# Kernel tuning notes

Hardware: AMD Instinct MI355X
Metric: run time of the kernel (lower is better)

Reference implementation:

```python
import jax, jax.numpy as jnp
import numpy as np

B, S, DM, H, D = 2, 1024, 1024, 16, 64  # batch, seq, d_model, heads, head_dim


def setup_inputs() -> dict:
    key = jax.random.key(0)
    ks = jax.random.split(key, 16)
    sc = 1.0 / np.sqrt(DM)
    scd = 1.0 / np.sqrt(D)
    return {
        "hidden_states": jax.random.normal(ks[0], (B, S, DM), dtype=jnp.float32),
        # frozen base_attn projections
        "Wq": jax.random.normal(ks[1], (DM, DM), dtype=jnp.float32) * sc,
        "bq": jnp.zeros((DM,), dtype=jnp.float32),
        "Wk": jax.random.normal(ks[2], (DM, DM), dtype=jnp.float32) * sc,
        "bk": jnp.zeros((DM,), dtype=jnp.float32),
        "Wv": jax.random.normal(ks[3], (DM, DM), dtype=jnp.float32) * sc,
        "bv": jnp.zeros((DM,), dtype=jnp.float32),
        "Wo": jax.random.normal(ks[4], (DM, DM), dtype=jnp.float32) * sc,
        "bo": jnp.zeros((DM,), dtype=jnp.float32),
        # trainable hedgehog feature maps (per-head Linear(head_dim, head_dim))
        "Wfq": jax.random.normal(ks[5], (D, D), dtype=jnp.float32) * scd,
        "bfq": jnp.zeros((D,), dtype=jnp.float32),
        "Wfk": jax.random.normal(ks[6], (D, D), dtype=jnp.float32) * scd,
        "bfk": jnp.zeros((D,), dtype=jnp.float32),
    }


def _heads(x):
    # (B, S, DM) -> (B, H, S, D)
    return x.reshape(B, S, H, D).transpose(0, 2, 1, 3)


def _feature_map(x, W, b):
    # HedgehogFeatureMap: Linear then concat(exp(x), exp(-x)) along last dim
    y = jnp.einsum('bhsd,ed->bhse', x, W) + b
    return jnp.concatenate([jnp.exp(y), jnp.exp(-y)], axis=-1)  # (B,H,S,2D)


def reference(hidden_states, Wq, bq, Wk, bk, Wv, bv, Wo, bo, Wfq, bfq, Wfk, bfk):
    # base_attn: standard multi-head softmax attention with output_attentions=True
    q = _heads(hidden_states @ Wq.T + bq)
    k = _heads(hidden_states @ Wk.T + bk)
    v = _heads(hidden_states @ Wv.T + bv)
    scores = jnp.einsum('bhmd,bhnd->bhmn', q, k) / jnp.sqrt(jnp.float32(D))
    true_attns = jax.nn.softmax(scores, axis=-1)  # (B,H,S,S)
    ctx = jnp.einsum('bhmn,bhnd->bhmd', true_attns, v)
    outputs = ctx.transpose(0, 2, 1, 3).reshape(B, S, DM) @ Wo.T + bo

    # hedgehog path: feature maps on q/k then sum-normalized quadratic attention
    fq = _feature_map(q, Wfq, bfq)
    fk = _feature_map(k, Wfk, bfk)
    qk = jnp.einsum('bhmd,bhnd->bhmn', fq, fk)
    pred_attns = qk / jnp.sum(qk, axis=-1, keepdims=True)
    return (outputs, pred_attns, true_attns)
```

## Files before the change

kernel.cpp:

```cpp
#include <hip/hip_runtime.h>
#include <math.h>

constexpr int B_ = 2, S_ = 1024, DM_ = 1024, NH_ = 16, HD_ = 64;
constexpr long SD = (long)S_ * DM_;
constexpr long SS = (long)S_ * S_;

typedef _Float16 half8 __attribute__((ext_vector_type(8)));
typedef _Float16 half4 __attribute__((ext_vector_type(4)));
typedef float floatx4 __attribute__((ext_vector_type(4)));

__device__ __forceinline__ void gl_lds16(const void* g, void* l) {
    __builtin_amdgcn_global_load_lds(
        (const __attribute__((address_space(1))) void*)g,
        (__attribute__((address_space(3))) void*)l, 16, 0, 0);
}

__global__ __launch_bounds__(256) void cvt_f2h(
    const float* __restrict__ x, _Float16* __restrict__ y, int n4)
{
    int i = (blockIdx.x * 256 + threadIdx.x);
    if (i < n4) {
        float4 v = ((const float4*)x)[i];
        half4 h = { (_Float16)v.x, (_Float16)v.y, (_Float16)v.z, (_Float16)v.w };
        ((half4*)y)[i] = h;
    }
}

template <int BM, int BN, int WM, int WN, int CONVA>
__global__ __launch_bounds__(256) void mm_nt(
    const void* __restrict__ Ap, const _Float16* __restrict__ Wp,
    const float* __restrict__ bias, const float* __restrict__ rowscale,
    float* __restrict__ Cf,
    _Float16* __restrict__ Ch, int K, int lda, int ldw, int ldc,
    long sAb, long sAh, long sWb, long sWh, long sCb, long sCh,
    float scale, int mode)
{
    constexpr int MI = WM / 16, NI = WN / 16;
    const int z = blockIdx.z, b = z / NH_, h = z % NH_;
    const int wave = threadIdx.x >> 6, lane = threadIdx.x & 63;
    const int m0 = blockIdx.y * BM, n0 = blockIdx.x * BN;
    const int wm = (wave >> 1) * WM, wn = (wave & 1) * WN;
    const int r16 = lane & 15, quad = lane >> 4;

    const _Float16* Wz = Wp + (long)b * sWb + (long)h * sWh;

    __shared__ __align__(16) _Float16 As[BM * 32];
    __shared__ __align__(16) _Float16 Bs[BN * 32];

    floatx4 acc[MI][NI];
#pragma unroll
    for (int i = 0; i < MI; ++i)
#pragma unroll
        for (int j = 0; j < NI; ++j)
#pragma unroll
            for (int r = 0; r < 4; ++r) acc[i][j][r] = 0.f;

    for (int k0 = 0; k0 < K; k0 += 32) {
        if constexpr (CONVA) {
            const float* Af = (const float*)Ap + (long)b * sAb + (long)h * sAh;
#pragma unroll
            for (int r = 0; r < BM / 32; ++r) {
                int idx = r * 1024 + threadIdx.x * 4;
                int row = idx >> 5, col = idx & 31;
                float4 v = *(const float4*)(Af + (long)(m0 + row) * lda + k0 + col);
                half4 hv = { (_Float16)v.x, (_Float16)v.y, (_Float16)v.z, (_Float16)v.w };
                *(half4*)&As[row * 32 + col] = hv;
            }
        } else {
            const _Float16* Ah = (const _Float16*)Ap + (long)b * sAb + (long)h * sAh;
#pragma unroll
            for (int c = wave * (BM / 64); c < (wave + 1) * (BM / 64); ++c) {
                const _Float16* g = Ah + (long)(m0 + c * 16 + (lane >> 2)) * lda
                                    + k0 + (lane & 3) * 8;
                gl_lds16(g, &As[c * 512]);
            }
        }
#pragma unroll
        for (int c = wave * (BN / 64); c < (wave + 1) * (BN / 64); ++c) {
            const _Float16* g = Wz + (long)(n0 + c * 16 + (lane >> 2)) * ldw
                                + k0 + (lane & 3) * 8;
            gl_lds16(g, &Bs[c * 512]);
        }
        __syncthreads();

        half8 af[MI], bf8[NI];
#pragma unroll
        for (int i = 0; i < MI; ++i)
            af[i] = *(const half8*)&As[(wm + i * 16 + r16) * 32 + quad * 8];
#pragma unroll
        for (int j = 0; j < NI; ++j)
            bf8[j] = *(const half8*)&Bs[(wn + j * 16 + r16) * 32 + quad * 8];
#pragma unroll
        for (int i = 0; i < MI; ++i)
#pragma unroll
            for (int j = 0; j < NI; ++j)
                acc[i][j] = __builtin_amdgcn_mfma_f32_16x16x32_f16(
                    af[i], bf8[j], acc[i][j], 0, 0, 0);
        __syncthreads();
    }

    const long cb = (long)b * sCb + (long)h * sCh;
#pragma unroll
    for (int i = 0; i < MI; ++i) {
#pragma unroll
        for (int j = 0; j < NI; ++j) {
#pragma unroll
            for (int r = 0; r < 4; ++r) {
                int row = m0 + wm + i * 16 + quad * 4 + r;
                int col = n0 + wn + j * 16 + r16;
                float v = acc[i][j][r] * scale;
                if (bias) v += bias[col];
                if (rowscale) v *= rowscale[(long)z * 1024 + row];
                if (mode == 0) Cf[cb + (long)row * ldc + col] = v;
                else           Ch[cb + (long)row * ldc + col] = (_Float16)v;
            }
        }
    }
}

__global__ __launch_bounds__(256) void qkv_proj(
    const _Float16* __restrict__ hsH,
    const _Float16* __restrict__ W0, const _Float16* __restrict__ W1,
    const _Float16* __restrict__ W2,
    const float* __restrict__ b0, const float* __restrict__ b1,
    const float* __restrict__ b2,
    _Float16* __restrict__ QH, _Float16* __restrict__ KH,
    _Float16* __restrict__ VtH)
{
    const int z = blockIdx.z;
    const _Float16* W = (z == 0) ? W0 : (z == 1) ? W1 : W2;
    const float* bias = (z == 0) ? b0 : (z == 1) ? b1 : b2;

    const int wave = threadIdx.x >> 6, lane = threadIdx.x & 63;
    const int m0 = blockIdx.y * 128, n0 = blockIdx.x * 128;
    const int wm = (wave >> 1) * 64, wn = (wave & 1) * 64;
    const int r16 = lane & 15, quad = lane >> 4;

    __shared__ __align__(16) _Float16 As[128 * 32];
    __shared__ __align__(16) _Float16 Bs[128 * 32];

    floatx4 acc[4][4];
#pragma unroll
    for (int i = 0; i < 4; ++i)
#pragma unroll
        for (int j = 0; j < 4; ++j)
#pragma unroll
            for (int r = 0; r < 4; ++r) acc[i][j][r] = 0.f;

    for (int k0 = 0; k0 < 1024; k0 += 32) {
#pragma unroll
        for (int c = wave * 2; c < wave * 2 + 2; ++c) {
            const _Float16* ga = hsH + (long)(m0 + c * 16 + (lane >> 2)) * 1024
                                 + k0 + (lane & 3) * 8;
            gl_lds16(ga, &As[c * 512]);
            const _Float16* gb = W + (long)(n0 + c * 16 + (lane >> 2)) * 1024
                                 + k0 + (lane & 3) * 8;
            gl_lds16(gb, &Bs[c * 512]);
        }
        __syncthreads();

        half8 af[4], bf8[4];
#pragma unroll
        for (int i = 0; i < 4; ++i)
            af[i] = *(const half8*)&As[(wm + i * 16 + r16) * 32 + quad * 8];
#pragma unroll
        for (int j = 0; j < 4; ++j)
            bf8[j] = *(const half8*)&Bs[(wn + j * 16 + r16) * 32 + quad * 8];
#pragma unroll
        for (int i = 0; i < 4; ++i)
#pragma unroll
            for (int j = 0; j < 4; ++j)
                acc[i][j] = __builtin_amdgcn_mfma_f32_16x16x32_f16(
                    af[i], bf8[j], acc[i][j], 0, 0, 0);
        __syncthreads();
    }

    _Float16* dst = (z == 0) ? QH : KH;
#pragma unroll
    for (int i = 0; i < 4; ++i) {
#pragma unroll
        for (int j = 0; j < 4; ++j) {
#pragma unroll
            for (int r = 0; r < 4; ++r) {
                int row = m0 + wm + i * 16 + quad * 4 + r;
                int col = n0 + wn + j * 16 + r16;
                float v = acc[i][j][r] + bias[col];
                if (z < 2) {
                    dst[(long)row * 1024 + col] = (_Float16)v;
                } else {
                    int bb = row >> 10, s = row & 1023;
                    int hh = col >> 6, d = col & 63;
                    VtH[((((long)bb * 16 + hh) * 64 + d) << 10) | s] = (_Float16)v;
                }
            }
        }
    }
}

__global__ __launch_bounds__(512) void attn_fused(
    const _Float16* __restrict__ Q, const _Float16* __restrict__ K,
    const _Float16* __restrict__ Vt, float* __restrict__ trueA,
    _Float16* __restrict__ ctx)
{
    const int z = blockIdx.y, b = z >> 4, h = z & 15;
    const int m0 = blockIdx.x * 32;
    const int wave = threadIdx.x >> 6, lane = threadIdx.x & 63;
    const int r16 = lane & 15, quad = lane >> 4;
    const int c0 = wave * 128;

    __shared__ __align__(16) _Float16 Ps[32 * 1024];
    float* redmx = (float*)Ps;
    float* redsm = (float*)Ps + 256;
    float* kred  = (float*)Ps;

    const _Float16* Qb = Q + (long)b * SD + h * 64;
    const _Float16* Kb = K + (long)b * SD + h * 64;

    half8 af[2][2];
#pragma unroll
    for (int mi = 0; mi < 2; ++mi)
#pragma unroll
        for (int ks = 0; ks < 2; ++ks)
            af[mi][ks] = *(const half8*)&Qb[(long)(m0 + mi * 16 + r16) * DM_
                                            + ks * 32 + quad * 8];

    floatx4 acc[2][8];
#pragma unroll
    for (int mi = 0; mi < 2; ++mi)
#pragma unroll
        for (int nj = 0; nj < 8; ++nj)
#pragma unroll
            for (int r = 0; r < 4; ++r) acc[mi][nj][r] = 0.f;

#pragma unroll
    for (int ks = 0; ks < 2; ++ks) {
#pragma unroll
        for (int nj = 0; nj < 8; ++nj) {
            half8 bf = *(const half8*)&Kb[(long)(c0 + nj * 16 + r16) * DM_
                                          + ks * 32 + quad * 8];
            acc[0][nj] = __builtin_amdgcn_mfma_f32_16x16x32_f16(
                af[0][ks], bf, acc[0][nj], 0, 0, 0);
            acc[1][nj] = __builtin_amdgcn_mfma_f32_16x16x32_f16(
                af[1][ks], bf, acc[1][nj], 0, 0, 0);
        }
    }

    float rmx[2][4];
#pragma unroll
    for (int mi = 0; mi < 2; ++mi)
#pragma unroll
        for (int r = 0; r < 4; ++r) {
            float m = acc[mi][0][r];
#pragma unroll
            for (int nj = 1; nj < 8; ++nj) m = fmaxf(m, acc[mi][nj][r]);
#pragma unroll
            for (int o = 1; o <= 8; o <<= 1) m = fmaxf(m, __shfl_xor(m, o, 64));
            rmx[mi][r] = m;
        }
    if (r16 == 0) {
#pragma unroll
        for (int mi = 0; mi < 2; ++mi)
#pragma unroll
            for (int r = 0; r < 4; ++r)
                redmx[wave * 32 + mi * 16 + quad * 4 + r] = rmx[mi][r];
    }
    __syncthreads();
    float mx[2][4];
#pragma unroll
    for (int mi = 0; mi < 2; ++mi)
#pragma unroll
        for (int r = 0; r < 4; ++r) {
            float m = redmx[mi * 16 + quad * 4 + r];
#pragma unroll
            for (int w = 1; w < 8; ++w)
                m = fmaxf(m, redmx[w * 32 + mi * 16 + quad * 4 + r]);
            mx[mi][r] = m;
        }

    float rsm[2][4];
#pragma unroll
    for (int mi = 0; mi < 2; ++mi)
#pragma unroll
        for (int r = 0; r < 4; ++r) {
            float s = 0.f;
#pragma unroll
            for (int nj = 0; nj < 8; ++nj) {
                float p = __expf((acc[mi][nj][r] - mx[mi][r]) * 0.125f);
                acc[mi][nj][r] = p;
                s += p;
            }
#pragma unroll
            for (int o = 1; o <= 8; o <<= 1) s += __shfl_xor(s, o, 64);
            rsm[mi][r] = s;
        }
    if (r16 == 0) {
#pragma unroll
        for (int mi = 0; mi < 2; ++mi)
#pragma unroll
            for (int r = 0; r < 4; ++r)
                redsm[wave * 32 + mi * 16 + quad * 4 + r] = rsm[mi][r];
    }
    __syncthreads();
    float inv[2][4];
#pragma unroll
    for (int mi = 0; mi < 2; ++mi)
#pragma unroll
        for (int r = 0; r < 4; ++r) {
            float s = 0.f;
#pragma unroll
            for (int w = 0; w < 8; ++w)
                s += redsm[w * 32 + mi * 16 + quad * 4 + r];
            inv[mi][r] = 1.f / s;
        }
    __syncthreads();

    float* Ta = trueA + (long)z * SS + (long)m0 * S_;
#pragma unroll
    for (int mi = 0; mi < 2; ++mi) {
#pragma unroll
        for (int r = 0; r < 4; ++r) {
            const int row = mi * 16 + quad * 4 + r;
            const int sw = (row & 7) << 3;
            const float iv = inv[mi][r];
#pragma unroll
            for (int nj = 0; nj < 8; ++nj) {
                const int col = c0 + nj * 16 + r16;
                const float v = acc[mi][nj][r] * iv;
                Ta[(long)row * S_ + col] = v;
                Ps[row * 1024 + (col ^ sw)] = (_Float16)v;
            }
        }
    }
    __syncthreads();

    const int d0 = (wave & 3) * 16, kr = wave >> 2;
    const _Float16* Vb = Vt + ((long)z * 64 + d0 + r16) * (long)S_;
    floatx4 c2[2];
#pragma unroll
    for (int mi = 0; mi < 2; ++mi)
#pragma unroll
        for (int r = 0; r < 4; ++r) c2[mi][r] = 0.f;

    const int swz = (r16 & 7) << 3;
#pragma unroll 4
    for (int k0 = kr * 512; k0 < kr * 512 + 512; k0 += 32) {
        half8 pa0 = *(const half8*)&Ps[r16 * 1024 + ((k0 + quad * 8) ^ swz)];
        half8 pa1 = *(const half8*)&Ps[(16 + r16) * 1024 + ((k0 + quad * 8) ^ swz)];
        half8 vf  = *(const half8*)&Vb[k0 + quad * 8];
        c2[0] = __builtin_amdgcn_mfma_f32_16x16x32_f16(pa0, vf, c2[0], 0, 0, 0);
        c2[1] = __builtin_amdgcn_mfma_f32_16x16x32_f16(pa1, vf, c2[1], 0, 0, 0);
    }

    __syncthreads();
    if (kr == 1) {
#pragma unroll
        for (int mi = 0; mi < 2; ++mi)
            *(floatx4*)&kred[(((wave & 3) * 2 + mi) * 64 + lane) * 4] = c2[mi];
    }
    __syncthreads();
    if (kr == 0) {
        _Float16* Cb = ctx + (long)b * SD + h * 64;
#pragma unroll
        for (int mi = 0; mi < 2; ++mi) {
            c2[mi] += *(const floatx4*)&kred[((wave * 2 + mi) * 64 + lane) * 4];
#pragma unroll
            for (int r = 0; r < 4; ++r) {
                const int srow = m0 + mi * 16 + quad * 4 + r;
                Cb[(long)srow * DM_ + d0 + r16] = (_Float16)c2[mi][r];
            }
        }
    }
}

__global__ __launch_bounds__(256) void feat_map(
    const _Float16* __restrict__ Xh, const _Float16* __restrict__ Wf,
    const float* __restrict__ bf, _Float16* __restrict__ outH)
{
    const int z = blockIdx.y, b = z >> 4, h = z & 15;
    const int m0 = blockIdx.x * 64;
    __shared__ float Xs[64][65];
    __shared__ float Ws[64][65];
    const _Float16* Xb = Xh + (long)b * SD + h * 64;
    for (int i = threadIdx.x; i < 4096; i += 256) {
        int r = i >> 6, c = i & 63;
        Xs[r][c] = (float)Xb[(long)(m0 + r) * 1024 + c];
        Ws[r][c] = (float)Wf[i];
    }
    __syncthreads();
    const int tm = (threadIdx.x >> 4) * 4, tn = (threadIdx.x & 15) * 4;
    float acc[4][4] = {{0.f}};
    for (int k = 0; k < 64; ++k) {
        float xv[4], wv[4];
#pragma unroll
        for (int i = 0; i < 4; ++i) xv[i] = Xs[tm + i][k];
#pragma unroll
        for (int j = 0; j < 4; ++j) wv[j] = Ws[tn + j][k];
#pragma unroll
        for (int i = 0; i < 4; ++i)
#pragma unroll
            for (int j = 0; j < 4; ++j) acc[i][j] = fmaf(xv[i], wv[j], acc[i][j]);
    }
#pragma unroll
    for (int i = 0; i < 4; ++i) {
        long base = ((long)z * S_ + m0 + tm + i) * 128;
#pragma unroll
        for (int j = 0; j < 4; ++j) {
            float y = acc[i][j] + bf[tn + j];
            outH[base + tn + j]      = (_Float16)expf(y);
            outH[base + 64 + tn + j] = (_Float16)expf(-y);
        }
    }
}

__global__ __launch_bounds__(256) void sum_fk(
    const _Float16* __restrict__ fkH, float* __restrict__ sk)
{
    const int z = blockIdx.x;
    const int col = threadIdx.x & 127, hlf = threadIdx.x >> 7;
    const _Float16* p = fkH + (long)z * S_ * 128 + (long)hlf * 512 * 128 + col;
    float s = 0.f;
    for (int i = 0; i < 512; ++i) s += (float)p[(long)i * 128];
    __shared__ float part[2][128];
    part[hlf][col] = s;
    __syncthreads();
    if (threadIdx.x < 128)
        sk[z * 128 + threadIdx.x] = part[0][threadIdx.x] + part[1][threadIdx.x];
}

__global__ __launch_bounds__(256) void rowsum_inv(
    const _Float16* __restrict__ fqH, const float* __restrict__ sk,
    float* __restrict__ rsinv)
{
    const int g = blockIdx.x * 256 + threadIdx.x;
    const int z = g >> 10;
    const _Float16* p = fqH + (long)g * 128;
    const float* s = sk + z * 128;
    float acc = 0.f;
#pragma unroll
    for (int d0 = 0; d0 < 128; d0 += 8) {
        half8 v = *(const half8*)(p + d0);
#pragma unroll
        for (int j = 0; j < 8; ++j) acc = fmaf((float)v[j], s[d0 + j], acc);
    }
    rsinv[g] = 1.f / acc;
}

extern "C" void kernel_launch(void* const* d_in, const int* in_sizes, int n_in,
                              void* d_out, int out_size, void* d_ws, size_t ws_size,
                              hipStream_t stream)
{
    (void)in_sizes; (void)n_in; (void)out_size; (void)ws_size;

    const float* hs  = (const float*)d_in[0];
    const float* Wq  = (const float*)d_in[1];
    const float* bq  = (const float*)d_in[2];
    const float* Wk  = (const float*)d_in[3];
    const float* bk  = (const float*)d_in[4];
    const float* Wv  = (const float*)d_in[5];
    const float* bv  = (const float*)d_in[6];
    const float* Wo  = (const float*)d_in[7];
    const float* bo  = (const float*)d_in[8];
    const float* Wfq = (const float*)d_in[9];
    const float* bfq = (const float*)d_in[10];
    const float* Wfk = (const float*)d_in[11];
    const float* bfk = (const float*)d_in[12];

    float* out0  = (float*)d_out;
    float* pred  = out0 + (long)B_ * S_ * DM_;
    float* trueA = pred + (long)B_ * NH_ * S_ * S_;

    _Float16* hsH  = (_Float16*)d_ws;
    _Float16* WqH  = hsH + 2 * 1024 * 1024;
    _Float16* WkH  = WqH + 1024 * 1024;
    _Float16* WvH  = WkH + 1024 * 1024;
    _Float16* WoH  = WvH + 1024 * 1024;
    _Float16* WfqH = WoH + 1024 * 1024;
    _Float16* WfkH = WfqH + 4096;
    _Float16* QH   = WfkH + 4096;
    _Float16* KH   = QH + 2 * 1024 * 1024;
    _Float16* VtH  = KH + 2 * 1024 * 1024;
    _Float16* ctxH = VtH + 2 * 1024 * 1024;
    _Float16* fqH  = ctxH + 2 * 1024 * 1024;
    _Float16* fkH  = fqH + (long)B_ * NH_ * S_ * 128;

    float* sk    = (float*)WqH;
    float* rsinv = sk + 32 * 128;

    const dim3 blk(256);

    cvt_f2h<<<2048, blk, 0, stream>>>(hs, hsH, 512 * 1024);
    cvt_f2h<<<1024, blk, 0, stream>>>(Wq, WqH, 256 * 1024);
    cvt_f2h<<<1024, blk, 0, stream>>>(Wk, WkH, 256 * 1024);
    cvt_f2h<<<1024, blk, 0, stream>>>(Wv, WvH, 256 * 1024);
    cvt_f2h<<<1024, blk, 0, stream>>>(Wo, WoH, 256 * 1024);
    cvt_f2h<<<4, blk, 0, stream>>>(Wfq, WfqH, 1024);
    cvt_f2h<<<4, blk, 0, stream>>>(Wfk, WfkH, 1024);

    qkv_proj<<<dim3(8, 16, 3), blk, 0, stream>>>(
        hsH, WqH, WkH, WvH, bq, bk, bv, QH, KH, VtH);

    attn_fused<<<dim3(32, 32), dim3(512), 0, stream>>>(
        QH, KH, VtH, trueA, ctxH);

    mm_nt<64, 128, 32, 64, 0><<<dim3(8, 32, 1), blk, 0, stream>>>(
        ctxH, WoH, bo, nullptr, out0, nullptr, 1024, 1024, 1024, 1024,
        0, 0, 0, 0, 0, 0, 1.f, 0);

    feat_map<<<dim3(16, 32), blk, 0, stream>>>(QH, WfqH, bfq, fqH);
    feat_map<<<dim3(16, 32), blk, 0, stream>>>(KH, WfkH, bfk, fkH);

    sum_fk<<<32, blk, 0, stream>>>(fkH, sk);
    rowsum_inv<<<128, blk, 0, stream>>>(fqH, sk, rsinv);

    mm_nt<128, 128, 64, 64, 0><<<dim3(8, 8, 32), blk, 0, stream>>>(
        fqH, fkH, nullptr, rsinv, pred, nullptr, 128, 128, 128, 1024,
        (long)16 * S_ * 128, (long)S_ * 128,
        (long)16 * S_ * 128, (long)S_ * 128,
        16 * SS, SS, 1.f, 0);
}
```

Baseline: 486.4 us.

## Merge conversion launches, fuse feature maps with key column sums, deepen GEMM K-step

Replaces seven fp32-to-fp16 conversion launches with one indexed kernel. Fuses the two feature-map launches into one grid and computes per-block partial column sums of the key features in its epilogue, which removes the separate sum_fk pass. rowsum_inv now reduces those partials itself. Both GEMM kernels load two 32-wide K slices per barrier (K step of 64), halving the number of synchronisations but doubling LDS use per block.

```diff
diff --git a/kernel.cpp b/kernel.cpp
--- a/kernel.cpp
+++ b/kernel.cpp
@@ -15,20 +15,33 @@
         (__attribute__((address_space(3))) void*)l, 16, 0, 0);
 }
 
-__global__ __launch_bounds__(256) void cvt_f2h(
-    const float* __restrict__ x, _Float16* __restrict__ y, int n4)
-{
-    int i = (blockIdx.x * 256 + threadIdx.x);
-    if (i < n4) {
-        float4 v = ((const float4*)x)[i];
-        half4 h = { (_Float16)v.x, (_Float16)v.y, (_Float16)v.z, (_Float16)v.w };
-        ((half4*)y)[i] = h;
-    }
-}
-
-template <int BM, int BN, int WM, int WN, int CONVA>
+__global__ __launch_bounds__(256) void cvt_all(
+    const float* __restrict__ hs,  const float* __restrict__ Wq,
+    const float* __restrict__ Wk,  const float* __restrict__ Wv,
+    const float* __restrict__ Wo,  const float* __restrict__ Wfq,
+    const float* __restrict__ Wfk,
+    _Float16* __restrict__ hsH, _Float16* __restrict__ WqH,
+    _Float16* __restrict__ WkH, _Float16* __restrict__ WvH,
+    _Float16* __restrict__ WoH, _Float16* __restrict__ WfqH,
+    _Float16* __restrict__ WfkH)
+{
+    long i = (long)blockIdx.x * 256 + threadIdx.x;
+    const float* src; _Float16* dst; long off;
+    if (i < 524288)       { src = hs;  dst = hsH;  off = i; }
+    else if (i < 786432)  { src = Wq;  dst = WqH;  off = i - 524288; }
+    else if (i < 1048576) { src = Wk;  dst = WkH;  off = i - 786432; }
+    else if (i < 1310720) { src = Wv;  dst = WvH;  off = i - 1048576; }
+    else if (i < 1572864) { src = Wo;  dst = WoH;  off = i - 1310720; }
+    else if (i < 1573888) { src = Wfq; dst = WfqH; off = i - 1572864; }
+    else                  { src = Wfk; dst = WfkH; off = i - 1573888; }
+    float4 v = ((const float4*)src)[off];
+    half4 h = { (_Float16)v.x, (_Float16)v.y, (_Float16)v.z, (_Float16)v.w };
+    ((half4*)dst)[off] = h;
+}
+
+template <int BM, int BN, int WM, int WN>
 __global__ __launch_bounds__(256) void mm_nt(
-    const void* __restrict__ Ap, const _Float16* __restrict__ Wp,
+    const _Float16* __restrict__ Ap, const _Float16* __restrict__ Wp,
     const float* __restrict__ bias, const float* __restrict__ rowscale,
     float* __restrict__ Cf,
     _Float16* __restrict__ Ch, int K, int lda, int ldw, int ldc,
@@ -42,10 +55,11 @@
     const int wm = (wave >> 1) * WM, wn = (wave & 1) * WN;
     const int r16 = lane & 15, quad = lane >> 4;
 
+    const _Float16* Az = Ap + (long)b * sAb + (long)h * sAh;
     const _Float16* Wz = Wp + (long)b * sWb + (long)h * sWh;
 
-    __shared__ __align__(16) _Float16 As[BM * 32];
-    __shared__ __align__(16) _Float16 Bs[BN * 32];
+    __shared__ __align__(16) _Float16 As[2 * BM * 32];
+    __shared__ __align__(16) _Float16 Bs[2 * BN * 32];
 
     floatx4 acc[MI][NI];
 #pragma unroll
@@ -55,47 +69,42 @@
 #pragma unroll
             for (int r = 0; r < 4; ++r) acc[i][j][r] = 0.f;
 
-    for (int k0 = 0; k0 < K; k0 += 32) {
-        if constexpr (CONVA) {
-            const float* Af = (const float*)Ap + (long)b * sAb + (long)h * sAh;
-#pragma unroll
-            for (int r = 0; r < BM / 32; ++r) {
-                int idx = r * 1024 + threadIdx.x * 4;
-                int row = idx >> 5, col = idx & 31;
-                float4 v = *(const float4*)(Af + (long)(m0 + row) * lda + k0 + col);
-                half4 hv = { (_Float16)v.x, (_Float16)v.y, (_Float16)v.z, (_Float16)v.w };
-                *(half4*)&As[row * 32 + col] = hv;
-            }
-        } else {
-            const _Float16* Ah = (const _Float16*)Ap + (long)b * sAb + (long)h * sAh;
+    for (int k0 = 0; k0 < K; k0 += 64) {
+#pragma unroll
+        for (int hf = 0; hf < 2; ++hf) {
 #pragma unroll
             for (int c = wave * (BM / 64); c < (wave + 1) * (BM / 64); ++c) {
-                const _Float16* g = Ah + (long)(m0 + c * 16 + (lane >> 2)) * lda
-                                    + k0 + (lane & 3) * 8;
-                gl_lds16(g, &As[c * 512]);
-            }
-        }
-#pragma unroll
-        for (int c = wave * (BN / 64); c < (wave + 1) * (BN / 64); ++c) {
-            const _Float16* g = Wz + (long)(n0 + c * 16 + (lane >> 2)) * ldw
-                                + k0 + (lane & 3) * 8;
-            gl_lds16(g, &Bs[c * 512]);
+                const _Float16* g = Az + (long)(m0 + c * 16 + (lane >> 2)) * lda
+                                    + k0 + hf * 32 + (lane & 3) * 8;
+                gl_lds16(g, &As[hf * BM * 32 + c * 512]);
+            }
+#pragma unroll
+            for (int c = wave * (BN / 64); c < (wave + 1) * (BN / 64); ++c) {
+                const _Float16* g = Wz + (long)(n0 + c * 16 + (lane >> 2)) * ldw
+                                    + k0 + hf * 32 + (lane & 3) * 8;
+                gl_lds16(g, &Bs[hf * BN * 32 + c * 512]);
+            }
         }
         __syncthreads();
 
-        half8 af[MI], bf8[NI];
-#pragma unroll
-        for (int i = 0; i < MI; ++i)
-            af[i] = *(const half8*)&As[(wm + i * 16 + r16) * 32 + quad * 8];
-#pragma unroll
-        for (int j = 0; j < NI; ++j)
-            bf8[j] = *(const half8*)&Bs[(wn + j * 16 + r16) * 32 + quad * 8];
-#pragma unroll
-        for (int i = 0; i < MI; ++i)
+#pragma unroll
+        for (int hf = 0; hf < 2; ++hf) {
+            half8 af[MI], bf8[NI];
+#pragma unroll
+            for (int i = 0; i < MI; ++i)
+                af[i] = *(const half8*)&As[hf * BM * 32
+                                           + (wm + i * 16 + r16) * 32 + quad * 8];
 #pragma unroll
             for (int j = 0; j < NI; ++j)
-                acc[i][j] = __builtin_amdgcn_mfma_f32_16x16x32_f16(
-                    af[i], bf8[j], acc[i][j], 0, 0, 0);
+                bf8[j] = *(const half8*)&Bs[hf * BN * 32
+                                            + (wn + j * 16 + r16) * 32 + quad * 8];
+#pragma unroll
+            for (int i = 0; i < MI; ++i)
+#pragma unroll
+                for (int j = 0; j < NI; ++j)
+                    acc[i][j] = __builtin_amdgcn_mfma_f32_16x16x32_f16(
+                        af[i], bf8[j], acc[i][j], 0, 0, 0);
+        }
         __syncthreads();
     }
 
@@ -136,8 +145,8 @@
     const int wm = (wave >> 1) * 64, wn = (wave & 1) * 64;
     const int r16 = lane & 15, quad = lane >> 4;
 
-    __shared__ __align__(16) _Float16 As[128 * 32];
-    __shared__ __align__(16) _Float16 Bs[128 * 32];
+    __shared__ __align__(16) _Float16 As[2 * 128 * 32];
+    __shared__ __align__(16) _Float16 Bs[2 * 128 * 32];
 
     floatx4 acc[4][4];
 #pragma unroll
@@ -147,31 +156,39 @@
 #pragma unroll
             for (int r = 0; r < 4; ++r) acc[i][j][r] = 0.f;
 
-    for (int k0 = 0; k0 < 1024; k0 += 32) {
-#pragma unroll
-        for (int c = wave * 2; c < wave * 2 + 2; ++c) {
-            const _Float16* ga = hsH + (long)(m0 + c * 16 + (lane >> 2)) * 1024
-                                 + k0 + (lane & 3) * 8;
-            gl_lds16(ga, &As[c * 512]);
-            const _Float16* gb = W + (long)(n0 + c * 16 + (lane >> 2)) * 1024
-                                 + k0 + (lane & 3) * 8;
-            gl_lds16(gb, &Bs[c * 512]);
+    for (int k0 = 0; k0 < 1024; k0 += 64) {
+#pragma unroll
+        for (int hf = 0; hf < 2; ++hf) {
+#pragma unroll
+            for (int c = wave * 2; c < wave * 2 + 2; ++c) {
+                const _Float16* ga = hsH + (long)(m0 + c * 16 + (lane >> 2)) * 1024
+                                     + k0 + hf * 32 + (lane & 3) * 8;
+                gl_lds16(ga, &As[hf * 4096 + c * 512]);
+                const _Float16* gb = W + (long)(n0 + c * 16 + (lane >> 2)) * 1024
+                                     + k0 + hf * 32 + (lane & 3) * 8;
+                gl_lds16(gb, &Bs[hf * 4096 + c * 512]);
+            }
         }
         __syncthreads();
 
-        half8 af[4], bf8[4];
-#pragma unroll
-        for (int i = 0; i < 4; ++i)
-            af[i] = *(const half8*)&As[(wm + i * 16 + r16) * 32 + quad * 8];
-#pragma unroll
-        for (int j = 0; j < 4; ++j)
-            bf8[j] = *(const half8*)&Bs[(wn + j * 16 + r16) * 32 + quad * 8];
-#pragma unroll
-        for (int i = 0; i < 4; ++i)
+#pragma unroll
+        for (int hf = 0; hf < 2; ++hf) {
+            half8 af[4], bf8[4];
+#pragma unroll
+            for (int i = 0; i < 4; ++i)
+                af[i] = *(const half8*)&As[hf * 4096
+                                           + (wm + i * 16 + r16) * 32 + quad * 8];
 #pragma unroll
             for (int j = 0; j < 4; ++j)
-                acc[i][j] = __builtin_amdgcn_mfma_f32_16x16x32_f16(
-                    af[i], bf8[j], acc[i][j], 0, 0, 0);
+                bf8[j] = *(const half8*)&Bs[hf * 4096
+                                            + (wn + j * 16 + r16) * 32 + quad * 8];
+#pragma unroll
+            for (int i = 0; i < 4; ++i)
+#pragma unroll
+                for (int j = 0; j < 4; ++j)
+                    acc[i][j] = __builtin_amdgcn_mfma_f32_16x16x32_f16(
+                        af[i], bf8[j], acc[i][j], 0, 0, 0);
+        }
         __syncthreads();
     }
 
@@ -372,14 +389,24 @@
     }
 }
 
-__global__ __launch_bounds__(256) void feat_map(
-    const _Float16* __restrict__ Xh, const _Float16* __restrict__ Wf,
-    const float* __restrict__ bf, _Float16* __restrict__ outH)
-{
+__global__ __launch_bounds__(256) void feat_map2(
+    const _Float16* __restrict__ QH, const _Float16* __restrict__ KH,
+    const _Float16* __restrict__ Wfq, const _Float16* __restrict__ Wfk,
+    const float* __restrict__ bfq, const float* __restrict__ bfk,
+    _Float16* __restrict__ fqH, _Float16* __restrict__ fkH,
+    float* __restrict__ skp)
+{
+    const int which = blockIdx.z;
+    const _Float16* Xh = which ? KH : QH;
+    const _Float16* Wf = which ? Wfk : Wfq;
+    const float* bf    = which ? bfk : bfq;
+    _Float16* outH     = which ? fkH : fqH;
+
     const int z = blockIdx.y, b = z >> 4, h = z & 15;
-    const int m0 = blockIdx.x * 64;
+    const int mb = blockIdx.x, m0 = mb * 64;
     __shared__ float Xs[64][65];
     __shared__ float Ws[64][65];
+    __shared__ float red[16][128];
     const _Float16* Xb = Xh + (long)b * SD + h * 64;
     for (int i = threadIdx.x; i < 4096; i += 256) {
         int r = i >> 6, c = i & 63;
@@ -387,7 +414,8 @@
         Ws[r][c] = (float)Wf[i];
     }
     __syncthreads();
-    const int tm = (threadIdx.x >> 4) * 4, tn = (threadIdx.x & 15) * 4;
+    const int tmg = threadIdx.x >> 4;
+    const int tm = tmg * 4, tn = (threadIdx.x & 15) * 4;
     float acc[4][4] = {{0.f}};
     for (int k = 0; k < 64; ++k) {
         float xv[4], wv[4];
@@ -400,47 +428,57 @@
 #pragma unroll
             for (int j = 0; j < 4; ++j) acc[i][j] = fmaf(xv[i], wv[j], acc[i][j]);
     }
+    float sp[4] = {0.f, 0.f, 0.f, 0.f}, sn[4] = {0.f, 0.f, 0.f, 0.f};
 #pragma unroll
     for (int i = 0; i < 4; ++i) {
         long base = ((long)z * S_ + m0 + tm + i) * 128;
 #pragma unroll
         for (int j = 0; j < 4; ++j) {
             float y = acc[i][j] + bf[tn + j];
-            outH[base + tn + j]      = (_Float16)expf(y);
-            outH[base + 64 + tn + j] = (_Float16)expf(-y);
-        }
-    }
-}
-
-__global__ __launch_bounds__(256) void sum_fk(
-    const _Float16* __restrict__ fkH, float* __restrict__ sk)
-{
-    const int z = blockIdx.x;
-    const int col = threadIdx.x & 127, hlf = threadIdx.x >> 7;
-    const _Float16* p = fkH + (long)z * S_ * 128 + (long)hlf * 512 * 128 + col;
-    float s = 0.f;
-    for (int i = 0; i < 512; ++i) s += (float)p[(long)i * 128];
-    __shared__ float part[2][128];
-    part[hlf][col] = s;
-    __syncthreads();
-    if (threadIdx.x < 128)
-        sk[z * 128 + threadIdx.x] = part[0][threadIdx.x] + part[1][threadIdx.x];
+            float ep = expf(y), en = expf(-y);
+            outH[base + tn + j]      = (_Float16)ep;
+            outH[base + 64 + tn + j] = (_Float16)en;
+            sp[j] += ep; sn[j] += en;
+        }
+    }
+    if (which) {
+#pragma unroll
+        for (int j = 0; j < 4; ++j) {
+            red[tmg][tn + j]      = sp[j];
+            red[tmg][64 + tn + j] = sn[j];
+        }
+        __syncthreads();
+        if (threadIdx.x < 128) {
+            float s = 0.f;
+#pragma unroll
+            for (int g = 0; g < 16; ++g) s += red[g][threadIdx.x];
+            skp[((long)z * 16 + mb) * 128 + threadIdx.x] = s;
+        }
+    }
 }
 
 __global__ __launch_bounds__(256) void rowsum_inv(
-    const _Float16* __restrict__ fqH, const float* __restrict__ sk,
+    const _Float16* __restrict__ fqH, const float* __restrict__ skp,
     float* __restrict__ rsinv)
 {
     const int g = blockIdx.x * 256 + threadIdx.x;
     const int z = g >> 10;
+    __shared__ float skz[128];
+    if (threadIdx.x < 128) {
+        float s = 0.f;
+#pragma unroll
+        for (int m = 0; m < 16; ++m)
+            s += skp[((long)z * 16 + m) * 128 + threadIdx.x];
+        skz[threadIdx.x] = s;
+    }
+    __syncthreads();
     const _Float16* p = fqH + (long)g * 128;
-    const float* s = sk + z * 128;
     float acc = 0.f;
 #pragma unroll
     for (int d0 = 0; d0 < 128; d0 += 8) {
         half8 v = *(const half8*)(p + d0);
 #pragma unroll
-        for (int j = 0; j < 8; ++j) acc = fmaf((float)v[j], s[d0 + j], acc);
+        for (int j = 0; j < 8; ++j) acc = fmaf((float)v[j], skz[d0 + j], acc);
     }
     rsinv[g] = 1.f / acc;
 }
@@ -483,18 +521,14 @@
     _Float16* fqH  = ctxH + 2 * 1024 * 1024;
     _Float16* fkH  = fqH + (long)B_ * NH_ * S_ * 128;
 
-    float* sk    = (float*)WqH;
-    float* rsinv = sk + 32 * 128;
+    float* skp   = (float*)WqH;
+    float* rsinv = (float*)WkH;
 
     const dim3 blk(256);
 
-    cvt_f2h<<<2048, blk, 0, stream>>>(hs, hsH, 512 * 1024);
-    cvt_f2h<<<1024, blk, 0, stream>>>(Wq, WqH, 256 * 1024);
-    cvt_f2h<<<1024, blk, 0, stream>>>(Wk, WkH, 256 * 1024);
-    cvt_f2h<<<1024, blk, 0, stream>>>(Wv, WvH, 256 * 1024);
-    cvt_f2h<<<1024, blk, 0, stream>>>(Wo, WoH, 256 * 1024);
-    cvt_f2h<<<4, blk, 0, stream>>>(Wfq, WfqH, 1024);
-    cvt_f2h<<<4, blk, 0, stream>>>(Wfk, WfkH, 1024);
+    cvt_all<<<6152, blk, 0, stream>>>(
+        hs, Wq, Wk, Wv, Wo, Wfq, Wfk,
+        hsH, WqH, WkH, WvH, WoH, WfqH, WfkH);
 
     qkv_proj<<<dim3(8, 16, 3), blk, 0, stream>>>(
         hsH, WqH, WkH, WvH, bq, bk, bv, QH, KH, VtH);
@@ -502,17 +536,16 @@
     attn_fused<<<dim3(32, 32), dim3(512), 0, stream>>>(
         QH, KH, VtH, trueA, ctxH);
 
-    mm_nt<64, 128, 32, 64, 0><<<dim3(8, 32, 1), blk, 0, stream>>>(
+    mm_nt<64, 128, 32, 64><<<dim3(8, 32, 1), blk, 0, stream>>>(
         ctxH, WoH, bo, nullptr, out0, nullptr, 1024, 1024, 1024, 1024,
         0, 0, 0, 0, 0, 0, 1.f, 0);
 
-    feat_map<<<dim3(16, 32), blk, 0, stream>>>(QH, WfqH, bfq, fqH);
-    feat_map<<<dim3(16, 32), blk, 0, stream>>>(KH, WfkH, bfk, fkH);
-
-    sum_fk<<<32, blk, 0, stream>>>(fkH, sk);
-    rowsum_inv<<<128, blk, 0, stream>>>(fqH, sk, rsinv);
-
-    mm_nt<128, 128, 64, 64, 0><<<dim3(8, 8, 32), blk, 0, stream>>>(
+    feat_map2<<<dim3(16, 32, 2), blk, 0, stream>>>(
+        QH, KH, WfqH, WfkH, bfq, bfk, fqH, fkH, skp);
+
+    rowsum_inv<<<128, blk, 0, stream>>>(fqH, skp, rsinv);
+
+    mm_nt<128, 128, 64, 64><<<dim3(8, 8, 32), blk, 0, stream>>>(
         fqH, fkH, nullptr, rsinv, pred, nullptr, 128, 128, 128, 1024,
         (long)16 * S_ * 128, (long)S_ * 128,
         (long)16 * S_ * 128, (long)S_ * 128,
```

Result: faster. 456.5 us (-6.2%).
